# Kernel tuning notes

Measured on AMD Instinct MI355X. Metric: run time of the kernel, lower is better.

## Reference

```python
import jax, jax.numpy as jnp
import numpy as np


def _axis_taps(g, size):
    # g: continuous grid coordinate; returns two neighbor indices (clamped)
    # and their linear interpolation weights, matching the HDRNet CUDA kernel:
    #   w = max(1 - |i + 0.5 - g|, 0)
    f = jnp.floor(g - 0.5)
    taps = []
    for off in (0.0, 1.0):
        idx = f + off
        w = jnp.maximum(1.0 - jnp.abs(idx + 0.5 - g), 0.0)
        i = jnp.clip(idx, 0, size - 1).astype(jnp.int32)
        taps.append((i, w))
    return taps


def bilateral_slice_apply(grid, guide, inp):
    # grid: [B, gh, gw, gd, n_out*(n_in+1)]   (has_offset=True)
    # guide: [B, H, W] in [0,1]
    # inp:  [B, H, W, n_in]
    B, gh, gw, gd, nc = grid.shape
    _, H, W, n_in = inp.shape
    n_out = nc // (n_in + 1)

    # continuous grid coords for each pixel / guide value
    gx = (jnp.arange(W, dtype=grid.dtype) + 0.5) * (gw / W)   # [W]
    gy = (jnp.arange(H, dtype=grid.dtype) + 0.5) * (gh / H)   # [H]
    gz = guide * gd                                           # [B,H,W]

    x_taps = _axis_taps(gx, gw)   # idx/w: [W]
    y_taps = _axis_taps(gy, gh)   # idx/w: [H]
    z_taps = _axis_taps(gz, gd)   # idx/w: [B,H,W]

    b = jnp.arange(B)[:, None, None]
    coeff = jnp.zeros((B, H, W, nc), dtype=grid.dtype)
    for yi, wy in y_taps:
        for xi, wx in x_taps:
            for zi, wz in z_taps:
                g = grid[b, yi[None, :, None], xi[None, None, :], zi]  # [B,H,W,nc]
                w = (wy[None, :, None] * wx[None, None, :] * wz)[..., None]
                coeff = coeff + w * g

    # per-pixel affine apply: out_o = sum_i A[o,i]*in_i + A[o,n_in]
    coeff = coeff.reshape(B, H, W, n_out, n_in + 1)
    out = jnp.einsum('bhwoc,bhwc->bhwo', coeff[..., :n_in], inp) + coeff[..., n_in]
    return out


def setup_inputs() -> dict:
    key = jax.random.key(0)
    k1, k2, k3 = jax.random.split(key, 3)
    B, gh, gw, gd = 4, 16, 16, 8
    H, W, n_in, n_out = 1024, 1024, 3, 3
    nc = n_out * (n_in + 1)  # has_offset=True -> 12
    grid = jax.random.normal(k1, (B, gh, gw, gd, nc), dtype=jnp.float32)
    guide = jax.random.uniform(k2, (B, H, W), dtype=jnp.float32)
    inp = jax.random.normal(k3, (B, H, W, n_in), dtype=jnp.float32)
    return {"grid": grid, "guide": guide, "input": inp}


def reference(grid, guide, input):
    return bilateral_slice_apply(grid, guide, input)
```

## Files before the change

### kernel.cpp

```cpp
#include <hip/hip_runtime.h>
#include <hip/hip_fp16.h>


struct __align__(16) H2x4 { __half2 x, y, z, w; };

__global__ __launch_bounds__(256, 4) void BilateralSliceApply_kernel(
    const float* __restrict__ grid,
    const float* __restrict__ guide,
    const float* __restrict__ inp,
    float* __restrict__ out)
{
    __shared__ H2x4 lA[24 * 64];
    __shared__ H2x4 lB[16 * 64];

    const int tx = blockIdx.x;
    const int ty = blockIdx.y;
    const int b  = blockIdx.z;
    const int t  = threadIdx.x;
    const int xl = t & 63;
    const int r0 = t >> 6;

    const int x0 = tx << 6;
    const int y0 = ty << 6;

    const int s0 = ty > 0 ? ty - 1 : 0;
    const int s1 = ty;
    const int s2 = ty < 15 ? ty + 1 : 15;

    const int pp0 = (((b << 10) + y0 + r0) << 10) + x0 + xl;
    float  gzA[8];
    float3 inA[8];
#pragma unroll
    for (int k = 0; k < 8; ++k) {
        const int pp = pp0 + (k << 12);
        gzA[k] = guide[pp];
        inA[k] = *(const float3*)(inp + (size_t)pp * 3);
    }

    const int fx  = (xl < 32) ? (tx - 1) : tx;
    const int ix0 = fx < 0 ? 0 : fx;
    const int ix1 = (fx + 1 > 15) ? 15 : fx + 1;
    const float wx1 = ((float)(x0 + xl) + 0.5f) * 0.015625f - 0.5f - (float)fx;
    const int bbase = b << 4;

    for (int L = r0; L < 40; L += 4) {
        const int z = L & 7;
        const int w = L >> 3;
        if (w < 3) {
            const int ycell = (w == 0) ? s0 : (w == 1 ? s1 : s2);
            const int cb = (bbase + ycell) << 4;
            const float* p0 = grid + (size_t)(((cb + ix0) << 3) + z) * 12;
            const float* p1 = grid + (size_t)(((cb + ix1) << 3) + z) * 12;
            const float4 a0 = *(const float4*)(p0 + 0);
            const float4 a1 = *(const float4*)(p0 + 4);
            const float4 b0 = *(const float4*)(p1 + 0);
            const float4 b1 = *(const float4*)(p1 + 4);
            H2x4 r;
            r.x = __floats2half2_rn(fmaf(wx1, b0.x - a0.x, a0.x),
                                    fmaf(wx1, b0.y - a0.y, a0.y));
            r.y = __floats2half2_rn(fmaf(wx1, b0.z - a0.z, a0.z),
                                    fmaf(wx1, b0.w - a0.w, a0.w));
            r.z = __floats2half2_rn(fmaf(wx1, b1.x - a1.x, a1.x),
                                    fmaf(wx1, b1.y - a1.y, a1.y));
            r.w = __floats2half2_rn(fmaf(wx1, b1.z - a1.z, a1.z),
                                    fmaf(wx1, b1.w - a1.w, a1.w));
            lA[(L << 6) + xl] = r;
        } else {
            const int v  = w - 3;
            const int pA = v ? s1 : s0;
            const int pB = v ? s2 : s1;
            const int cbA = (bbase + pA) << 4;
            const int cbB = (bbase + pB) << 4;
            const float4 a0 = *(const float4*)(grid + (size_t)(((cbA + ix0) << 3) + z) * 12 + 8);
            const float4 a1 = *(const float4*)(grid + (size_t)(((cbA + ix1) << 3) + z) * 12 + 8);
            const float4 b0 = *(const float4*)(grid + (size_t)(((cbB + ix0) << 3) + z) * 12 + 8);
            const float4 b1 = *(const float4*)(grid + (size_t)(((cbB + ix1) << 3) + z) * 12 + 8);
            H2x4 r;
            r.x = __floats2half2_rn(fmaf(wx1, a1.x - a0.x, a0.x),
                                    fmaf(wx1, a1.y - a0.y, a0.y));
            r.y = __floats2half2_rn(fmaf(wx1, a1.z - a0.z, a0.z),
                                    fmaf(wx1, a1.w - a0.w, a0.w));
            r.z = __floats2half2_rn(fmaf(wx1, b1.x - b0.x, b0.x),
                                    fmaf(wx1, b1.y - b0.y, b0.y));
            r.w = __floats2half2_rn(fmaf(wx1, b1.z - b0.z, b0.z),
                                    fmaf(wx1, b1.w - b0.w, b0.w));
            lB[((L - 24) << 6) + xl] = r;
        }
    }
    __syncthreads();

    float  gzB[8];
    float3 inB[8];
#pragma unroll
    for (int k = 0; k < 8; ++k) {
        const int pp = pp0 + ((k + 8) << 12);
        gzB[k] = guide[pp];
        inB[k] = *(const float3*)(inp + (size_t)pp * 3);
    }

#pragma unroll
    for (int k = 0; k < 16; ++k) {
        const int v   = k >> 3;
        const int row = r0 + (k << 2);
        const int pp  = pp0 + (k << 12);

        const float wy1 = ((float)row + 0.5f) * 0.015625f + (v ? -0.5f : 0.5f);
        const float wy0 = 1.0f - wy1;

        const float gz  = (v ? gzB[k - 8] : gzA[k]) * 8.0f;
        const float fz  = floorf(gz - 0.5f);
        const float wz1 = gz - 0.5f - fz;
        const float wz0 = 1.0f - wz1;
        const int ifz = (int)fz;
        const int iz0 = ifz < 0 ? 0 : (ifz > 7 ? 7 : ifz);
        const int nz  = ifz + 1;
        const int iz1 = nz < 0 ? 0 : (nz > 7 ? 7 : nz);

        const __half2 hA0 = __float2half2_rn(wy0 * wz0);
        const __half2 hA1 = __float2half2_rn(wy0 * wz1);
        const __half2 hB0 = __float2half2_rn(wy1 * wz0);
        const __half2 hB1 = __float2half2_rn(wy1 * wz1);

        const int slotLo = v;
        const int slotHi = v + 1;

        const H2x4 vA00 = lA[(((slotLo << 3) + iz0) << 6) + xl];
        const H2x4 vA01 = lA[(((slotLo << 3) + iz1) << 6) + xl];
        const H2x4 vA10 = lA[(((slotHi << 3) + iz0) << 6) + xl];
        const H2x4 vA11 = lA[(((slotHi << 3) + iz1) << 6) + xl];
        const H2x4 vB0  = lB[(((v << 3) + iz0) << 6) + xl];
        const H2x4 vB1  = lB[(((v << 3) + iz1) << 6) + xl];

        __half2 q0 = __hmul2(hA0, vA00.x);
        __half2 q1 = __hmul2(hA0, vA00.y);
        __half2 q2 = __hmul2(hA0, vA00.z);
        __half2 q3 = __hmul2(hA0, vA00.w);
        q0 = __hfma2(hA1, vA01.x, q0);
        q1 = __hfma2(hA1, vA01.y, q1);
        q2 = __hfma2(hA1, vA01.z, q2);
        q3 = __hfma2(hA1, vA01.w, q3);
        q0 = __hfma2(hB0, vA10.x, q0);
        q1 = __hfma2(hB0, vA10.y, q1);
        q2 = __hfma2(hB0, vA10.z, q2);
        q3 = __hfma2(hB0, vA10.w, q3);
        q0 = __hfma2(hB1, vA11.x, q0);
        q1 = __hfma2(hB1, vA11.y, q1);
        q2 = __hfma2(hB1, vA11.z, q2);
        q3 = __hfma2(hB1, vA11.w, q3);

        __half2 q4 = __hmul2(hA0, vB0.x);
        __half2 q5 = __hmul2(hA0, vB0.y);
        q4 = __hfma2(hA1, vB1.x, q4);
        q5 = __hfma2(hA1, vB1.y, q5);
        q4 = __hfma2(hB0, vB0.z, q4);
        q5 = __hfma2(hB0, vB0.w, q5);
        q4 = __hfma2(hB1, vB1.z, q4);
        q5 = __hfma2(hB1, vB1.w, q5);

        const float3 in = v ? inB[k - 8] : inA[k];
        const __half2 i01 = __floats2half2_rn(in.x, in.y);
        const __half2 i21 = __floats2half2_rn(in.z, 1.0f);

        __half2 r0h = __hmul2(q0, i01); r0h = __hfma2(q1, i21, r0h);
        __half2 r1h = __hmul2(q2, i01); r1h = __hfma2(q3, i21, r1h);
        __half2 r2h = __hmul2(q4, i01); r2h = __hfma2(q5, i21, r2h);

        float3 o;
        o.x = __low2float(r0h) + __high2float(r0h);
        o.y = __low2float(r1h) + __high2float(r1h);
        o.z = __low2float(r2h) + __high2float(r2h);
        *(float3*)(out + (size_t)pp * 3) = o;
    }
}

extern "C" void kernel_launch(void* const* d_in, const int* in_sizes, int n_in,
                              void* d_out, int out_size, void* d_ws, size_t ws_size,
                              hipStream_t stream) {
    const float* grid  = (const float*)d_in[0];
    const float* guide = (const float*)d_in[1];
    const float* inp   = (const float*)d_in[2];
    float* out = (float*)d_out;

    dim3 gridDim(16, 16, 4);
    BilateralSliceApply_kernel<<<gridDim, 256, 0, stream>>>(grid, guide, inp, out);
}
```

Before: 117.0 us.

## Shrink tiles to 16 rows so each block uses a single y-cell pair

Result: slower. 121.8 us (+4.1%).

```diff
diff --git a/kernel.cpp b/kernel.cpp
--- a/kernel.cpp
+++ b/kernel.cpp
@@ -4,37 +4,37 @@
 
 struct __align__(16) H2x4 { __half2 x, y, z, w; };
 
-__global__ __launch_bounds__(256, 4) void BilateralSliceApply_kernel(
+__global__ __launch_bounds__(256, 6) void BilateralSliceApply_kernel(
     const float* __restrict__ grid,
     const float* __restrict__ guide,
     const float* __restrict__ inp,
     float* __restrict__ out)
 {
-    __shared__ H2x4 lA[24 * 64];
-    __shared__ H2x4 lB[16 * 64];
+    __shared__ H2x4 lA[16 * 64];
+    __shared__ H2x4 lB[ 8 * 64];
 
-    const int tx = blockIdx.x;
-    const int ty = blockIdx.y;
-    const int b  = blockIdx.z;
-    const int t  = threadIdx.x;
-    const int xl = t & 63;
-    const int r0 = t >> 6;
+    const int tx  = blockIdx.x;
+    const int tyt = blockIdx.y;
+    const int b   = blockIdx.z;
+    const int t   = threadIdx.x;
+    const int xl  = t & 63;
+    const int r0  = t >> 6;
 
     const int x0 = tx << 6;
-    const int y0 = ty << 6;
+    const int y0 = tyt << 4;
 
-    const int s0 = ty > 0 ? ty - 1 : 0;
-    const int s1 = ty;
-    const int s2 = ty < 15 ? ty + 1 : 15;
+    const int fy  = (y0 < 32) ? -1 : ((y0 - 32) >> 6);
+    const int ycA = fy < 0 ? 0 : fy;
+    const int ycB = (fy + 1 > 15) ? 15 : fy + 1;
 
     const int pp0 = (((b << 10) + y0 + r0) << 10) + x0 + xl;
-    float  gzA[8];
-    float3 inA[8];
+    float  gz4[4];
+    float3 in4[4];
 #pragma unroll
-    for (int k = 0; k < 8; ++k) {
+    for (int k = 0; k < 4; ++k) {
         const int pp = pp0 + (k << 12);
-        gzA[k] = guide[pp];
-        inA[k] = *(const float3*)(inp + (size_t)pp * 3);
+        gz4[k] = guide[pp];
+        in4[k] = *(const float3*)(inp + (size_t)pp * 3);
     }
 
     const int fx  = (xl < 32) ? (tx - 1) : tx;
@@ -43,11 +43,11 @@
     const float wx1 = ((float)(x0 + xl) + 0.5f) * 0.015625f - 0.5f - (float)fx;
     const int bbase = b << 4;
 
-    for (int L = r0; L < 40; L += 4) {
+    for (int L = r0; L < 24; L += 4) {
         const int z = L & 7;
-        const int w = L >> 3;
-        if (w < 3) {
-            const int ycell = (w == 0) ? s0 : (w == 1 ? s1 : s2);
+        if (L < 16) {
+            const int yc = L >> 3;
+            const int ycell = yc ? ycB : ycA;
             const int cb = (bbase + ycell) << 4;
             const float* p0 = grid + (size_t)(((cb + ix0) << 3) + z) * 12;
             const float* p1 = grid + (size_t)(((cb + ix1) << 3) + z) * 12;
@@ -66,11 +66,8 @@
                                     fmaf(wx1, b1.w - a1.w, a1.w));
             lA[(L << 6) + xl] = r;
         } else {
-            const int v  = w - 3;
-            const int pA = v ? s1 : s0;
-            const int pB = v ? s2 : s1;
-            const int cbA = (bbase + pA) << 4;
-            const int cbB = (bbase + pB) << 4;
+            const int cbA = (bbase + ycA) << 4;
+            const int cbB = (bbase + ycB) << 4;
             const float4 a0 = *(const float4*)(grid + (size_t)(((cbA + ix0) << 3) + z) * 12 + 8);
             const float4 a1 = *(const float4*)(grid + (size_t)(((cbA + ix1) << 3) + z) * 12 + 8);
             const float4 b0 = *(const float4*)(grid + (size_t)(((cbB + ix0) << 3) + z) * 12 + 8);
@@ -84,30 +81,21 @@
                                     fmaf(wx1, b1.y - b0.y, b0.y));
             r.w = __floats2half2_rn(fmaf(wx1, b1.z - b0.z, b0.z),
                                     fmaf(wx1, b1.w - b0.w, b0.w));
-            lB[((L - 24) << 6) + xl] = r;
+            lB[(z << 6) + xl] = r;
         }
     }
     __syncthreads();
 
-    float  gzB[8];
-    float3 inB[8];
+    const float wybase = (float)y0 * 0.015625f - 0.5f - (float)fy;
 #pragma unroll
-    for (int k = 0; k < 8; ++k) {
-        const int pp = pp0 + ((k + 8) << 12);
-        gzB[k] = guide[pp];
-        inB[k] = *(const float3*)(inp + (size_t)pp * 3);
-    }
-
-#pragma unroll
-    for (int k = 0; k < 16; ++k) {
-        const int v   = k >> 3;
+    for (int k = 0; k < 4; ++k) {
         const int row = r0 + (k << 2);
         const int pp  = pp0 + (k << 12);
 
-        const float wy1 = ((float)row + 0.5f) * 0.015625f + (v ? -0.5f : 0.5f);
+        const float wy1 = wybase + ((float)row + 0.5f) * 0.015625f;
         const float wy0 = 1.0f - wy1;
 
-        const float gz  = (v ? gzB[k - 8] : gzA[k]) * 8.0f;
+        const float gz  = gz4[k] * 8.0f;
         const float fz  = floorf(gz - 0.5f);
         const float wz1 = gz - 0.5f - fz;
         const float wz0 = 1.0f - wz1;
@@ -121,15 +109,12 @@
         const __half2 hB0 = __float2half2_rn(wy1 * wz0);
         const __half2 hB1 = __float2half2_rn(wy1 * wz1);
 
-        const int slotLo = v;
-        const int slotHi = v + 1;
-
-        const H2x4 vA00 = lA[(((slotLo << 3) + iz0) << 6) + xl];
-        const H2x4 vA01 = lA[(((slotLo << 3) + iz1) << 6) + xl];
-        const H2x4 vA10 = lA[(((slotHi << 3) + iz0) << 6) + xl];
-        const H2x4 vA11 = lA[(((slotHi << 3) + iz1) << 6) + xl];
-        const H2x4 vB0  = lB[(((v << 3) + iz0) << 6) + xl];
-        const H2x4 vB1  = lB[(((v << 3) + iz1) << 6) + xl];
+        const H2x4 vA00 = lA[(iz0 << 6) + xl];
+        const H2x4 vA01 = lA[(iz1 << 6) + xl];
+        const H2x4 vA10 = lA[((8 + iz0) << 6) + xl];
+        const H2x4 vA11 = lA[((8 + iz1) << 6) + xl];
+        const H2x4 vB0  = lB[(iz0 << 6) + xl];
+        const H2x4 vB1  = lB[(iz1 << 6) + xl];
 
         __half2 q0 = __hmul2(hA0, vA00.x);
         __half2 q1 = __hmul2(hA0, vA00.y);
@@ -157,7 +142,7 @@
         q4 = __hfma2(hB1, vB1.z, q4);
         q5 = __hfma2(hB1, vB1.w, q5);
 
-        const float3 in = v ? inB[k - 8] : inA[k];
+        const float3 in = in4[k];
         const __half2 i01 = __floats2half2_rn(in.x, in.y);
         const __half2 i21 = __floats2half2_rn(in.z, 1.0f);
 
@@ -181,6 +166,6 @@
     const float* inp   = (const float*)d_in[2];
     float* out = (float*)d_out;
 
-    dim3 gridDim(16, 16, 4);
+    dim3 gridDim(16, 64, 4);
     BilateralSliceApply_kernel<<<gridDim, 256, 0, stream>>>(grid, guide, inp, out);
 }
```

## Align row tiles to grid-cell y-intervals and stage raw grid cells in LDS

Applied to the files above, without the earlier changes.

New measurement: 147.1 us. +25.7%, slower.

```diff
diff --git a/kernel.cpp b/kernel.cpp
--- a/kernel.cpp
+++ b/kernel.cpp
@@ -4,30 +4,45 @@
 
 struct __align__(16) H2x4 { __half2 x, y, z, w; };
 
-__global__ __launch_bounds__(256, 4) void BilateralSliceApply_kernel(
+__global__ __launch_bounds__(256, 6) void BilateralSliceApply_kernel(
     const float* __restrict__ grid,
     const float* __restrict__ guide,
     const float* __restrict__ inp,
     float* __restrict__ out)
 {
-    __shared__ H2x4 lA[24 * 64];
-    __shared__ H2x4 lB[16 * 64];
+    __shared__ float lraw[576];
+    __shared__ H2x4  lA[16 * 64];
+    __shared__ H2x4  lB[ 8 * 64];
 
     const int tx = blockIdx.x;
-    const int ty = blockIdx.y;
+    const int g  = blockIdx.y;
     const int b  = blockIdx.z;
     const int t  = threadIdx.x;
     const int xl = t & 63;
     const int r0 = t >> 6;
 
-    const int x0 = tx << 6;
-    const int y0 = ty << 6;
+    const int x0     = tx << 6;
+    const int ystart = (g == 0) ? 0 : ((g << 6) - 32);
+    const int interior = (g != 0) & (g != 16);
 
-    const int s0 = ty > 0 ? ty - 1 : 0;
-    const int s1 = ty;
-    const int s2 = ty < 15 ? ty + 1 : 15;
+    const int fy  = g - 1;
+    const int ycA = fy < 0 ? 0 : fy;
+    const int ycB = g > 15 ? 15 : g;
 
-    const int pp0 = (((b << 10) + y0 + r0) << 10) + x0 + xl;
+    const int bb16 = b << 4;
+    for (int d = t; d < 576; d += 256) {
+        const int yc  = d >= 288 ? 1 : 0;
+        const int rem = d - (yc ? 288 : 0);
+        const int xco = rem / 96;
+        const int wi  = rem - xco * 96;
+        int cx = tx - 1 + xco;
+        cx = cx < 0 ? 0 : (cx > 15 ? 15 : cx);
+        const int yce = yc ? ycB : ycA;
+        lraw[d] = grid[(size_t)(((bb16 + yce) << 4) + cx) * 96 + wi];
+    }
+    __syncthreads();
+
+    const int pp0 = (((b << 10) + ystart + r0) << 10) + x0 + xl;
     float  gzA[8];
     float3 inA[8];
 #pragma unroll
@@ -38,23 +53,20 @@
     }
 
     const int fx  = (xl < 32) ? (tx - 1) : tx;
-    const int ix0 = fx < 0 ? 0 : fx;
-    const int ix1 = (fx + 1 > 15) ? 15 : fx + 1;
     const float wx1 = ((float)(x0 + xl) + 0.5f) * 0.015625f - 0.5f - (float)fx;
-    const int bbase = b << 4;
+    const int cb = (xl < 32) ? 0 : 96;
 
-    for (int L = r0; L < 40; L += 4) {
+#pragma unroll
+    for (int q = 0; q < 6; ++q) {
+        const int L = r0 + (q << 2);
         const int z = L & 7;
-        const int w = L >> 3;
-        if (w < 3) {
-            const int ycell = (w == 0) ? s0 : (w == 1 ? s1 : s2);
-            const int cb = (bbase + ycell) << 4;
-            const float* p0 = grid + (size_t)(((cb + ix0) << 3) + z) * 12;
-            const float* p1 = grid + (size_t)(((cb + ix1) << 3) + z) * 12;
-            const float4 a0 = *(const float4*)(p0 + 0);
-            const float4 a1 = *(const float4*)(p0 + 4);
-            const float4 b0 = *(const float4*)(p1 + 0);
-            const float4 b1 = *(const float4*)(p1 + 4);
+        if (L < 16) {
+            const int yc   = L >> 3;
+            const int base = yc * 288 + cb + z * 12;
+            const float4 a0 = *(const float4*)&lraw[base];
+            const float4 a1 = *(const float4*)&lraw[base + 4];
+            const float4 b0 = *(const float4*)&lraw[base + 96];
+            const float4 b1 = *(const float4*)&lraw[base + 100];
             H2x4 r;
             r.x = __floats2half2_rn(fmaf(wx1, b0.x - a0.x, a0.x),
                                     fmaf(wx1, b0.y - a0.y, a0.y));
@@ -66,48 +78,45 @@
                                     fmaf(wx1, b1.w - a1.w, a1.w));
             lA[(L << 6) + xl] = r;
         } else {
-            const int v  = w - 3;
-            const int pA = v ? s1 : s0;
-            const int pB = v ? s2 : s1;
-            const int cbA = (bbase + pA) << 4;
-            const int cbB = (bbase + pB) << 4;
-            const float4 a0 = *(const float4*)(grid + (size_t)(((cbA + ix0) << 3) + z) * 12 + 8);
-            const float4 a1 = *(const float4*)(grid + (size_t)(((cbA + ix1) << 3) + z) * 12 + 8);
-            const float4 b0 = *(const float4*)(grid + (size_t)(((cbB + ix0) << 3) + z) * 12 + 8);
-            const float4 b1 = *(const float4*)(grid + (size_t)(((cbB + ix1) << 3) + z) * 12 + 8);
+            const int base = cb + z * 12 + 8;
+            const float4 aA = *(const float4*)&lraw[base];
+            const float4 bA = *(const float4*)&lraw[base + 96];
+            const float4 aB = *(const float4*)&lraw[base + 288];
+            const float4 bB = *(const float4*)&lraw[base + 384];
             H2x4 r;
-            r.x = __floats2half2_rn(fmaf(wx1, a1.x - a0.x, a0.x),
-                                    fmaf(wx1, a1.y - a0.y, a0.y));
-            r.y = __floats2half2_rn(fmaf(wx1, a1.z - a0.z, a0.z),
-                                    fmaf(wx1, a1.w - a0.w, a0.w));
-            r.z = __floats2half2_rn(fmaf(wx1, b1.x - b0.x, b0.x),
-                                    fmaf(wx1, b1.y - b0.y, b0.y));
-            r.w = __floats2half2_rn(fmaf(wx1, b1.z - b0.z, b0.z),
-                                    fmaf(wx1, b1.w - b0.w, b0.w));
-            lB[((L - 24) << 6) + xl] = r;
+            r.x = __floats2half2_rn(fmaf(wx1, bA.x - aA.x, aA.x),
+                                    fmaf(wx1, bA.y - aA.y, aA.y));
+            r.y = __floats2half2_rn(fmaf(wx1, bA.z - aA.z, aA.z),
+                                    fmaf(wx1, bA.w - aA.w, aA.w));
+            r.z = __floats2half2_rn(fmaf(wx1, bB.x - aB.x, aB.x),
+                                    fmaf(wx1, bB.y - aB.y, aB.y));
+            r.w = __floats2half2_rn(fmaf(wx1, bB.z - aB.z, aB.z),
+                                    fmaf(wx1, bB.w - aB.w, aB.w));
+            lB[(z << 6) + xl] = r;
         }
     }
     __syncthreads();
 
     float  gzB[8];
     float3 inB[8];
+    if (interior) {
 #pragma unroll
-    for (int k = 0; k < 8; ++k) {
-        const int pp = pp0 + ((k + 8) << 12);
-        gzB[k] = guide[pp];
-        inB[k] = *(const float3*)(inp + (size_t)pp * 3);
+        for (int k = 0; k < 8; ++k) {
+            const int pp = pp0 + ((k + 8) << 12);
+            gzB[k] = guide[pp];
+            inB[k] = *(const float3*)(inp + (size_t)pp * 3);
+        }
     }
 
-#pragma unroll
-    for (int k = 0; k < 16; ++k) {
-        const int v   = k >> 3;
-        const int row = r0 + (k << 2);
-        const int pp  = pp0 + (k << 12);
+    const float wybase = ((float)(ystart + r0) + 0.5f) * 0.015625f - 0.5f - (float)fy;
+    const int nk = interior ? 16 : 8;
+    for (int k = 0; k < nk; ++k) {
+        const int pp = pp0 + (k << 12);
 
-        const float wy1 = ((float)row + 0.5f) * 0.015625f + (v ? -0.5f : 0.5f);
+        const float wy1 = wybase + (float)(k << 2) * 0.015625f;
         const float wy0 = 1.0f - wy1;
 
-        const float gz  = (v ? gzB[k - 8] : gzA[k]) * 8.0f;
+        const float gz  = (k < 8 ? gzA[k & 7] : gzB[k & 7]) * 8.0f;
         const float fz  = floorf(gz - 0.5f);
         const float wz1 = gz - 0.5f - fz;
         const float wz0 = 1.0f - wz1;
@@ -121,15 +130,12 @@
         const __half2 hB0 = __float2half2_rn(wy1 * wz0);
         const __half2 hB1 = __float2half2_rn(wy1 * wz1);
 
-        const int slotLo = v;
-        const int slotHi = v + 1;
-
-        const H2x4 vA00 = lA[(((slotLo << 3) + iz0) << 6) + xl];
-        const H2x4 vA01 = lA[(((slotLo << 3) + iz1) << 6) + xl];
-        const H2x4 vA10 = lA[(((slotHi << 3) + iz0) << 6) + xl];
-        const H2x4 vA11 = lA[(((slotHi << 3) + iz1) << 6) + xl];
-        const H2x4 vB0  = lB[(((v << 3) + iz0) << 6) + xl];
-        const H2x4 vB1  = lB[(((v << 3) + iz1) << 6) + xl];
+        const H2x4 vA00 = lA[(iz0 << 6) + xl];
+        const H2x4 vA01 = lA[(iz1 << 6) + xl];
+        const H2x4 vA10 = lA[((8 + iz0) << 6) + xl];
+        const H2x4 vA11 = lA[((8 + iz1) << 6) + xl];
+        const H2x4 vB0  = lB[(iz0 << 6) + xl];
+        const H2x4 vB1  = lB[(iz1 << 6) + xl];
 
         __half2 q0 = __hmul2(hA0, vA00.x);
         __half2 q1 = __hmul2(hA0, vA00.y);
@@ -157,7 +163,7 @@
         q4 = __hfma2(hB1, vB1.z, q4);
         q5 = __hfma2(hB1, vB1.w, q5);
 
-        const float3 in = v ? inB[k - 8] : inA[k];
+        const float3 in = (k < 8) ? inA[k & 7] : inB[k & 7];
         const __half2 i01 = __floats2half2_rn(in.x, in.y);
         const __half2 i21 = __floats2half2_rn(in.z, 1.0f);
 
@@ -181,6 +187,6 @@
     const float* inp   = (const float*)d_in[2];
     float* out = (float*)d_out;
 
-    dim3 gridDim(16, 16, 4);
+    dim3 gridDim(16, 17, 4);
     BilateralSliceApply_kernel<<<gridDim, 256, 0, stream>>>(grid, guide, inp, out);
 }
```
